# Kernel tuning notes

Hardware: AMD Instinct MI355X
Metric: run time of the kernel (lower is better)

Reference implementation:

```python
import math
import jax, jax.numpy as jnp
import numpy as np

B, H, L = 8, 512, 4096
N = 64 // 2  # d_state//2 complex pairs
DT_MIN, DT_MAX = 1e-3, 0.1


def setup_inputs() -> dict:
    key = jax.random.key(0)
    k_u, k_dt, k_C, k_D, k_W = jax.random.split(key, 5)
    u = jax.random.normal(k_u, (B, H, L), dtype=jnp.float32)
    log_dt = jax.random.uniform(k_dt, (H,), dtype=jnp.float32) * (
        math.log(DT_MAX) - math.log(DT_MIN)) + math.log(DT_MIN)
    log_A_real = jnp.log(0.5 * jnp.ones((H, N), dtype=jnp.float32))
    A_imag = math.pi * jnp.broadcast_to(jnp.arange(N, dtype=jnp.float32), (H, N))
    C = jax.random.normal(k_C, (H, N, 2), dtype=jnp.float32)  # view_as_real of cfloat
    D = jax.random.normal(k_D, (H,), dtype=jnp.float32)
    W_out = jax.random.normal(k_W, (2 * H, H), dtype=jnp.float32) * 0.05  # 1x1 conv weight
    b_out = jnp.zeros((2 * H,), dtype=jnp.float32)
    return {"u": u, "log_dt": log_dt, "log_A_real": log_A_real, "A_imag": A_imag,
            "C": C, "D": D, "W_out": W_out, "b_out": b_out}


def _ssm_kernel(log_dt, log_A_real, A_imag, C, length):
    dt = jnp.exp(log_dt)                             # (H,)
    A = -jnp.exp(log_A_real) + 1j * A_imag           # (H,N) complex
    dtA = A * dt[:, None]                            # (H,N)
    l = jnp.arange(length, dtype=jnp.float32)
    K = jnp.exp(dtA[:, :, None] * l)                 # (H,N,L) complex Vandermonde
    Cc = C[..., 0] + 1j * C[..., 1]                  # (H,N)
    Cs = Cc * (jnp.exp(dtA) - 1.0) / A               # (H,N)
    return 2.0 * jnp.einsum('hn,hnl->hl', Cs, K).real  # (H,L) real kernel


def reference(u, log_dt, log_A_real, A_imag, C, D, W_out, b_out):
    length = u.shape[-1]
    k = _ssm_kernel(log_dt, log_A_real, A_imag, C, length)  # (H,L)
    n_fft = 2 * length
    k_f = jnp.fft.rfft(k, n=n_fft)                   # (H, L+1)
    u_f = jnp.fft.rfft(u, n=n_fft)                   # (B,H,L+1)
    y = jnp.fft.irfft(u_f * k_f, n=n_fft)[..., :length]  # FFT convolution
    y = y + u * D[:, None]                           # D skip connection
    y = jax.nn.gelu(y, approximate=False)            # torch nn.GELU = exact erf
    y = jnp.einsum('oh,bhl->bol', W_out, y) + b_out[:, None]  # 1x1 conv
    a, b = jnp.split(y, 2, axis=-2)                  # GLU over channel dim
    return a * jax.nn.sigmoid(b)
```

## Files before the change

### kernel.cpp

```cpp
#include <hip/hip_runtime.h>
#include <math.h>

constexpr int cB = 8, cH = 512, cL = 4096, cN = 32;
constexpr int cG = 32, cLC = 128;
constexpr int cHN = cH * cN;

constexpr size_t OF_RR  = 0;
constexpr size_t OF_RI  = (size_t)cHN;
constexpr size_t OF_RPR = (size_t)2*cHN;
constexpr size_t OF_RPI = (size_t)3*cHN;
constexpr size_t OF_C2R = (size_t)4*cHN;
constexpr size_t OF_C2I = (size_t)5*cHN;
constexpr size_t OF_DR  = (size_t)6*cHN;
constexpr size_t OF_DI  = (size_t)7*cHN;
constexpr size_t OF_K   = (size_t)8*cHN;
constexpr size_t OF_WP  = OF_K + (size_t)512*128;
constexpr size_t OF_A   = OF_WP + (size_t)1024*512/2;
constexpr size_t OF_V   = OF_A + (size_t)512*128*192/2;
constexpr size_t OF_XP  = OF_V + (size_t)512*64*128/2;
constexpr size_t OF_G   = OF_XP + (size_t)512*256*64/2;
constexpr size_t OF_GT  = OF_A;

typedef __bf16 bf16x8 __attribute__((ext_vector_type(8)));
typedef float  f32x4  __attribute__((ext_vector_type(4)));

static __device__ __forceinline__ ushort f2bf(float x) {
    unsigned u = __float_as_uint(x);
    unsigned r = (u + 0x7fffu + ((u >> 16) & 1u)) >> 16;
    return (ushort)r;
}
static __device__ __forceinline__ float bf2f(ushort v) {
    return __uint_as_float(((unsigned)v) << 16);
}
static __device__ __forceinline__ unsigned pk2(float a, float b) {
    return (unsigned)f2bf(a) | ((unsigned)f2bf(b) << 16);
}
static __device__ __forceinline__ float gelu(float v) {
    return 0.5f * v * (1.0f + erff(v * 0.70710678118654752f));
}
static __device__ __forceinline__ void gload16(const void* g, void* l) {
    __builtin_amdgcn_global_load_lds(
        (const __attribute__((address_space(1))) unsigned*)g,
        (__attribute__((address_space(3))) unsigned*)l, 16, 0, 0);
}

__global__ void k_consts_vmat(const float* __restrict__ log_dt,
                              const float* __restrict__ log_A_real,
                              const float* __restrict__ A_imag,
                              const float* __restrict__ Cin,
                              float* __restrict__ ws,
                              ushort* __restrict__ wsu)
{
    int tid = blockIdx.x * 256 + threadIdx.x;
    if (tid >= cHN) return;
    int h = tid >> 5, n = tid & 31;
    float dt = expf(log_dt[h]);
    float Ar = -expf(log_A_real[tid]);
    float Ai = A_imag[tid];
    float dr = dt * Ar, di = dt * Ai;
    float er = expf(dr);
    float rr = er * cosf(di), ri = er * sinf(di);
    float erL = expf(dr * (float)cLC);
    float diL = di * (float)cLC;
    float rpr = erL * cosf(diL), rpi = erL * sinf(diL);
    float cr = Cin[2*tid], ci = Cin[2*tid+1];
    float nr = rr - 1.0f, ni = ri;
    float inv = 1.0f / (Ar*Ar + Ai*Ai);
    float wr = (nr*Ar + ni*Ai) * inv;
    float wi = (ni*Ar - nr*Ai) * inv;
    float csr = cr*wr - ci*wi;
    float csi = cr*wi + ci*wr;
    ws[OF_RR  + tid] = rr;  ws[OF_RI  + tid] = ri;
    ws[OF_RPR + tid] = rpr; ws[OF_RPI + tid] = rpi;
    ws[OF_C2R + tid] = 2.0f*csr; ws[OF_C2I + tid] = 2.0f*csi;
    ws[OF_DR  + tid] = dr;  ws[OF_DI  + tid] = di;

    float e127 = expf(dr * 127.f), a127 = di * 127.f;
    float pr = e127 * cosf(a127), pi_ = e127 * sinf(a127);
    float rie = expf(-dr);
    float rc = rie * cosf(di), rs = -rie * sinf(di);
    ushort* vre = wsu + 2*OF_V + ((size_t)h*64 + n) * 128;
    ushort* vim = wsu + 2*OF_V + ((size_t)h*64 + 32 + n) * 128;
    for (int j4 = 0; j4 < 128; j4 += 4) {
        ushort4 r4, i4;
        #pragma unroll
        for (int e = 0; e < 4; ++e) {
            ((ushort*)&r4)[e] = f2bf(pr);
            ((ushort*)&i4)[e] = f2bf(pi_);
            float npr = pr*rc - pi_*rs;
            float npi = pr*rs + pi_*rc;
            pr = npr; pi_ = npi;
        }
        *(ushort4*)&vre[j4] = r4;
        *(ushort4*)&vim[j4] = i4;
    }
}

__global__ void k_pack_w(const float* __restrict__ W, ushort* __restrict__ Wp)
{
    int idx = blockIdx.x * 256 + threadIdx.x;
    int base = idx * 4;
    int m = base >> 9;
    int k = base & 511;
    int src = (m & 1) ? (512 + (m >> 1)) : (m >> 1);
    float4 v = *(const float4*)&W[(size_t)src * 512 + k];
    ushort4 o;
    o.x = f2bf(v.x); o.y = f2bf(v.y); o.z = f2bf(v.z); o.w = f2bf(v.w);
    *(ushort4*)&Wp[base] = o;
}

__global__ void k_embt(const float* __restrict__ ws, const float* __restrict__ Dvec,
                       ushort* __restrict__ wsu)
{
    __shared__ float kv[256];
    int t = threadIdx.x;
    int tid = blockIdx.x * 256 + t;
    int h = tid >> 7, l = tid & 127;
    float fl = (float)l, fl1 = (float)(l + 1);
    const float* dr_ = ws + OF_DR + (size_t)h*32;
    const float* di_ = ws + OF_DI + (size_t)h*32;
    const float* c2r_ = ws + OF_C2R + (size_t)h*32;
    const float* c2i_ = ws + OF_C2I + (size_t)h*32;
    ushort* rowA = wsu + 2*OF_A + ((size_t)h*128 + l) * 192;
    float kacc = 0.f;
    for (int n4 = 0; n4 < 32; n4 += 4) {
        ushort4 prq, npq;
        #pragma unroll
        for (int e = 0; e < 4; ++e) {
            int n = n4 + e;
            float dr = dr_[n], di = di_[n], c2r = c2r_[n], c2i = c2i_[n];
            float e0 = expf(dr * fl), a0 = di * fl;
            float c0 = cosf(a0), s0 = sinf(a0);
            kacc += e0 * (c2r*c0 - c2i*s0);
            float e1 = expf(dr * fl1), a1 = di * fl1;
            float c1 = cosf(a1), s1 = sinf(a1);
            ((ushort*)&prq)[e] = f2bf(e1 * (c2r*c1 - c2i*s1));
            ((ushort*)&npq)[e] = f2bf(-e1 * (c2r*s1 + c2i*c1));
        }
        *(ushort4*)&rowA[128 + n4] = prq;
        *(ushort4*)&rowA[160 + n4] = npq;
    }
    kv[t] = kacc;
    __syncthreads();
    const float* krow = kv + ((t >> 7) << 7);
    float Dh = Dvec[h];
    for (int j8 = 0; j8 < 128; j8 += 8) {
        uint4 q;
        unsigned w[4];
        #pragma unroll
        for (int p = 0; p < 4; ++p) {
            int j0 = j8 + 2*p, j1 = j0 + 1;
            float v0 = (j0 <= l) ? krow[l - j0] : 0.f;
            float v1 = (j1 <= l) ? krow[l - j1] : 0.f;
            if (j0 == l) v0 += Dh;
            if (j1 == l) v1 += Dh;
            w[p] = pk2(v0, v1);
        }
        q.x = w[0]; q.y = w[1]; q.z = w[2]; q.w = w[3];
        *(uint4*)&rowA[j8] = q;
    }
}

__global__ __launch_bounds__(256) void k_state_gemm(const float* __restrict__ u,
                                                    const ushort* __restrict__ wsu,
                                                    ushort* __restrict__ xp)
{
    __shared__ ushort Vs[64 * 136];
    __shared__ ushort Bs[256 * 40];
    const int t = threadIdx.x;
    const int h = blockIdx.x;
    const int wn = t >> 6, lane = t & 63;
    const int lm = lane & 15, q = lane >> 4;

    {
        int idx = t * 32;
        int row = idx >> 7, kk = idx & 127;
        const ushort* src = wsu + 2*OF_V + ((size_t)h*64 + row) * 128 + kk;
        uint4 v0 = *(const uint4*)&src[0],  v1 = *(const uint4*)&src[8];
        uint4 v2 = *(const uint4*)&src[16], v3 = *(const uint4*)&src[24];
        ushort* d = (ushort*)Vs + row * 136 + kk;
        *(uint4*)&d[0] = v0; *(uint4*)&d[8] = v1;
        *(uint4*)&d[16] = v2; *(uint4*)&d[24] = v3;
    }

    const int b = t >> 5, c = t & 31;
    f32x4 acc[4][4];
    #pragma unroll
    for (int i = 0; i < 4; ++i)
        #pragma unroll
        for (int j = 0; j < 4; ++j) acc[i][j] = (f32x4){0.f,0.f,0.f,0.f};

    for (int k0 = 0; k0 < 128; k0 += 32) {
        const float* up = u + ((size_t)(b*cH + h)) * cL + (size_t)c*128 + k0;
        float4 f[8];
        #pragma unroll
        for (int e = 0; e < 8; ++e) f[e] = *(const float4*)&up[4*e];
        __syncthreads();
        ushort* d = (ushort*)Bs + t * 40;
        #pragma unroll
        for (int e = 0; e < 4; ++e) {
            uint4 w;
            w.x = pk2(f[2*e].x, f[2*e].y);   w.y = pk2(f[2*e].z, f[2*e].w);
            w.z = pk2(f[2*e+1].x, f[2*e+1].y); w.w = pk2(f[2*e+1].z, f[2*e+1].w);
            *(uint4*)&d[8*e] = w;
        }
        __syncthreads();
        bf16x8 af[4], bfr[4];
        #pragma unroll
        for (int mi = 0; mi < 4; ++mi)
            af[mi] = *(const bf16x8*)&Vs[(16*mi + lm) * 136 + k0 + 8*q];
        #pragma unroll
        for (int ni = 0; ni < 4; ++ni)
            bfr[ni] = *(const bf16x8*)&Bs[(64*wn + 16*ni + lm) * 40 + 8*q];
        #pragma unroll
        for (int mi = 0; mi < 4; ++mi)
            #pragma unroll
            for (int ni = 0; ni < 4; ++ni)
                acc[mi][ni] = __builtin_amdgcn_mfma_f32_16x16x32_bf16(af[mi], bfr[ni], acc[mi][ni], 0,0,0);
    }
    #pragma unroll
    for (int mi = 0; mi < 4; ++mi)
        #pragma unroll
        for (int ni = 0; ni < 4; ++ni) {
            int col = 64*wn + 16*ni + lm;
            int comp = 16*mi + 4*q;
            ushort4 st;
            st.x = f2bf(acc[mi][ni][0]); st.y = f2bf(acc[mi][ni][1]);
            st.z = f2bf(acc[mi][ni][2]); st.w = f2bf(acc[mi][ni][3]);
            *(ushort4*)&xp[((size_t)h*256 + col) * 64 + comp] = st;
        }
}

__global__ __launch_bounds__(256) void k_scan2(const float* __restrict__ ws,
                                               ushort* __restrict__ xp)
{
    int tid = blockIdx.x * 256 + threadIdx.x;
    int n  = tid & 31;
    int bh = tid >> 5;
    int h  = bh & (cH - 1);
    int b  = bh >> 9;
    float rpr = ws[OF_RPR + (size_t)h*32 + n];
    float rpi = ws[OF_RPI + (size_t)h*32 + n];
    float Xr = 0.f, Xi = 0.f;
    ushort* base = xp + ((size_t)h*256 + (size_t)b*32) * 64 + n;
    for (int c = 0; c < cG; ++c) {
        ushort* p = base + (size_t)c * 64;
        float sr = bf2f(p[0]), si = bf2f(p[32]);
        p[0]  = f2bf(Xr);
        p[32] = f2bf(Xi);
        float nXr = fmaf(rpr, Xr, fmaf(-rpi, Xi, sr));
        float nXi = fmaf(rpr, Xi, fmaf(rpi, Xr, si));
        Xr = nXr; Xi = nXi;
    }
}

__global__ __launch_bounds__(256) void k_conv(const float* __restrict__ u,
                                              const ushort* __restrict__ wsu,
                                              ushort* __restrict__ g)
{
    __shared__ ushort As[128 * 40];
    __shared__ ushort Bs[128 * 40];
    const int t = threadIdx.x;
    const int ctile = blockIdx.x;
    const int h = blockIdx.y;
    const int wave = t >> 6, lane = t & 63;
    const int wm = wave & 1, wn = wave >> 1;
    const int lm = lane & 15, q = lane >> 4;

    const int arow = t & 127, ah = t >> 7;
    const int col = arow, half = ah;
    const int gc = ctile * 128 + col;
    const int ub = gc >> 5, uc = gc & 31;

    const ushort* Ab = wsu + 2*OF_A + ((size_t)h*128 + arow) * 192;
    const ushort* xpB = wsu + 2*OF_XP + ((size_t)h*256 + gc) * 64;

    f32x4 acc[4][4];
    #pragma unroll
    for (int i = 0; i < 4; ++i)
        #pragma unroll
        for (int j = 0; j < 4; ++j) acc[i][j] = (f32x4){0.f,0.f,0.f,0.f};

    for (int k0 = 0; k0 < 192; k0 += 32) {
        uint4 a0 = *(const uint4*)&Ab[k0 + 16*ah];
        uint4 a1 = *(const uint4*)&Ab[k0 + 16*ah + 8];
        uint4 b0, b1;
        if (k0 < 128) {
            const float* up = u + ((size_t)(ub*cH + h)) * cL + (size_t)uc*128 + k0 + 16*half;
            float4 f0 = *(const float4*)&up[0],  f1 = *(const float4*)&up[4];
            float4 f2 = *(const float4*)&up[8],  f3 = *(const float4*)&up[12];
            b0.x = pk2(f0.x,f0.y); b0.y = pk2(f0.z,f0.w);
            b0.z = pk2(f1.x,f1.y); b0.w = pk2(f1.z,f1.w);
            b1.x = pk2(f2.x,f2.y); b1.y = pk2(f2.z,f2.w);
            b1.z = pk2(f3.x,f3.y); b1.w = pk2(f3.z,f3.w);
        } else {
            const ushort* xs = xpB + (k0 - 128) + 16*half;
            b0 = *(const uint4*)&xs[0];
            b1 = *(const uint4*)&xs[8];
        }
        __syncthreads();
        *(uint4*)&As[arow*40 + 16*ah]     = a0;
        *(uint4*)&As[arow*40 + 16*ah + 8] = a1;
        *(uint4*)&Bs[col*40 + 16*half]     = b0;
        *(uint4*)&Bs[col*40 + 16*half + 8] = b1;
        __syncthreads();
        bool skip = (wm == 0) && (k0 == 64 || k0 == 96);
        if (!skip) {
            bf16x8 af[4], bfr[4];
            #pragma unroll
            for (int mi = 0; mi < 4; ++mi)
                af[mi] = *(const bf16x8*)&As[(64*wm + 16*mi + lm) * 40 + 8*q];
            #pragma unroll
            for (int ni = 0; ni < 4; ++ni)
                bfr[ni] = *(const bf16x8*)&Bs[(64*wn + 16*ni + lm) * 40 + 8*q];
            #pragma unroll
            for (int mi = 0; mi < 4; ++mi)
                #pragma unroll
                for (int ni = 0; ni < 4; ++ni)
                    acc[mi][ni] = __builtin_amdgcn_mfma_f32_16x16x32_bf16(af[mi], bfr[ni], acc[mi][ni], 0,0,0);
        }
    }
    #pragma unroll
    for (int ni = 0; ni < 4; ++ni) {
        int ocol = ctile*128 + 64*wn + 16*ni + lm;
        int ob = ocol >> 5, oc = ocol & 31;
        ushort* grow = g + ((size_t)(ob*cH + h)) * cL + (size_t)oc*128;
        #pragma unroll
        for (int mi = 0; mi < 4; ++mi) {
            int l = 64*wm + 16*mi + 4*q;
            ushort4 st;
            st.x = f2bf(gelu(acc[mi][ni][0]));
            st.y = f2bf(gelu(acc[mi][ni][1]));
            st.z = f2bf(gelu(acc[mi][ni][2]));
            st.w = f2bf(gelu(acc[mi][ni][3]));
            *(ushort4*)&grow[l] = st;
        }
    }
}

__global__ __launch_bounds__(256) void k_transpose(const ushort* __restrict__ gsrc,
                                                   ushort* __restrict__ gT)
{
    __shared__ ushort tile[64 * 64];
    const int t = threadIdx.x;
    const int b  = blockIdx.z;
    const int h0 = blockIdx.y << 6;
    const int l0 = blockIdx.x << 6;
    const ushort* gb = gsrc + ((size_t)b * cH + h0) * cL + l0;
    const int lb = t & 7;
    #pragma unroll
    for (int half = 0; half < 2; ++half) {
        int r = (t >> 3) + half * 32;
        uint4 v = *(const uint4*)&gb[(size_t)r * cL + lb * 8];
        int sb = lb ^ (r & 7) ^ (r >> 3);
        *(uint4*)&tile[r * 64 + sb * 8] = v;
    }
    __syncthreads();
    ushort* gTb = gT + ((size_t)b * cL + l0) * cH + h0;
    #pragma unroll
    for (int half = 0; half < 2; ++half) {
        int l  = (t >> 3) + half * 32;
        int hb = t & 7;
        ushort vals[8];
        #pragma unroll
        for (int e = 0; e < 8; ++e) {
            int r  = hb * 8 + e;
            int sb = (l >> 3) ^ (r & 7) ^ (r >> 3);
            vals[e] = tile[r * 64 + sb * 8 + (l & 7)];
        }
        *(uint4*)&gTb[(size_t)l * cH + hb * 8] = *(uint4*)vals;
    }
}

__global__ __launch_bounds__(256) void k_gemm2(const ushort* __restrict__ Wp,
                                               const float* __restrict__ bias,
                                               const ushort* __restrict__ gT,
                                               float* __restrict__ out)
{
    __shared__ ushort As[3][128 * 32];
    __shared__ ushort Bs[3][128 * 32];
    const int t    = threadIdx.x;
    const int l0   = blockIdx.x * 128;
    const int by   = blockIdx.y;
    const int b    = blockIdx.z;
    const int wave = t >> 6, lane = t & 63;
    const int wm   = wave & 1, wn = wave >> 1;
    const int lm   = lane & 15, q = lane >> 4;

    const int srow  = lane >> 2;
    const int sw_st = (((lane & 3) ^ ((srow >> 1) & 3)) * 8);
    const int sw_rd = ((q ^ ((lm >> 1) & 3)) * 8);
    const ushort* Ag = Wp + (size_t)(by * 128) * 512;
    const ushort* Bg = gT + ((size_t)b * cL + l0) * 512;

    f32x4 acc[4][4];
    #pragma unroll
    for (int i = 0; i < 4; ++i)
        #pragma unroll
        for (int j = 0; j < 4; ++j)
            acc[i][j] = (f32x4){0.f, 0.f, 0.f, 0.f};

    auto stage = [&](int bi, int kt) {
        const int k0 = kt * 32;
        #pragma unroll
        for (int j = 0; j < 2; ++j) {
            int row = 32*wave + 16*j + srow;
            gload16(Ag + (size_t)row * 512 + k0 + sw_st,
                    (char*)&As[bi][0] + wave*2048 + j*1024);
            gload16(Bg + (size_t)row * 512 + k0 + sw_st,
                    (char*)&Bs[bi][0] + wave*2048 + j*1024);
        }
    };
    auto compute = [&](int bi) {
        bf16x8 af[4], bfr[4];
        #pragma unroll
        for (int mi = 0; mi < 4; ++mi)
            af[mi] = *(const bf16x8*)&As[bi][(64*wm + 16*mi + lm) * 32 + sw_rd];
        #pragma unroll
        for (int ni = 0; ni < 4; ++ni)
            bfr[ni] = *(const bf16x8*)&Bs[bi][(64*wn + 16*ni + lm) * 32 + sw_rd];
        #pragma unroll
        for (int mi = 0; mi < 4; ++mi)
            #pragma unroll
            for (int ni = 0; ni < 4; ++ni)
                acc[mi][ni] = __builtin_amdgcn_mfma_f32_16x16x32_bf16(af[mi], bfr[ni], acc[mi][ni], 0,0,0);
    };

    stage(0, 0);
    stage(1, 1);
    int c0 = 0, c1 = 1, c2 = 2;
    for (int ks = 0; ks < 14; ++ks) {
        stage(c2, ks + 2);
        asm volatile("s_waitcnt vmcnt(8)" ::: "memory");
        __builtin_amdgcn_s_barrier();
        asm volatile("" ::: "memory");
        __builtin_amdgcn_sched_barrier(0);
        compute(c0);
        asm volatile("" ::: "memory");
        __builtin_amdgcn_sched_barrier(0);
        __builtin_amdgcn_s_barrier();
        int tmp = c0; c0 = c1; c1 = c2; c2 = tmp;
    }
    asm volatile("s_waitcnt vmcnt(4)" ::: "memory");
    __builtin_amdgcn_s_barrier();
    asm volatile("" ::: "memory");
    __builtin_amdgcn_sched_barrier(0);
    compute(c0);
    asm volatile("s_waitcnt vmcnt(0)" ::: "memory");
    __builtin_amdgcn_s_barrier();
    asm volatile("" ::: "memory");
    __builtin_amdgcn_sched_barrier(0);
    compute(c1);

    const int obase = by * 64 + 32 * wm;
    #pragma unroll
    for (int mi = 0; mi < 4; ++mi) {
        #pragma unroll
        for (int p = 0; p < 2; ++p) {
            int o = obase + 8*mi + 2*q + p;
            float ba = bias[o], bb = bias[512 + o];
            float* orow = out + ((size_t)b * cH + o) * cL + l0 + 64*wn + lm;
            #pragma unroll
            for (int ni = 0; ni < 4; ++ni) {
                float av = acc[mi][ni][2*p]     + ba;
                float gv = acc[mi][ni][2*p + 1] + bb;
                orow[16 * ni] = av / (1.f + expf(-gv));
            }
        }
    }
}

extern "C" void kernel_launch(void* const* d_in, const int* in_sizes, int n_in,
                              void* d_out, int out_size, void* d_ws, size_t ws_size,
                              hipStream_t stream)
{
    (void)in_sizes; (void)n_in; (void)out_size; (void)ws_size;
    const float* u          = (const float*)d_in[0];
    const float* log_dt     = (const float*)d_in[1];
    const float* log_A_real = (const float*)d_in[2];
    const float* A_imag     = (const float*)d_in[3];
    const float* C          = (const float*)d_in[4];
    const float* D          = (const float*)d_in[5];
    const float* W          = (const float*)d_in[6];
    const float* bias       = (const float*)d_in[7];
    float* out = (float*)d_out;
    float* ws  = (float*)d_ws;
    ushort* wsu = (ushort*)d_ws;
    ushort* Wp  = wsu + 2*OF_WP;
    ushort* xp  = wsu + 2*OF_XP;
    ushort* gbf = wsu + 2*OF_G;
    ushort* gTu = wsu + 2*OF_GT;

    hipLaunchKernelGGL(k_consts_vmat, dim3(cHN/256), dim3(256), 0, stream,
                       log_dt, log_A_real, A_imag, C, ws, wsu);
    hipLaunchKernelGGL(k_pack_w, dim3(1024*512/4/256), dim3(256), 0, stream, W, Wp);
    hipLaunchKernelGGL(k_embt, dim3(512*128/256), dim3(256), 0, stream, ws, D, wsu);
    hipLaunchKernelGGL(k_state_gemm, dim3(512), dim3(256), 0, stream, u, wsu, xp);
    hipLaunchKernelGGL(k_scan2, dim3(cB*cH*cN/256), dim3(256), 0, stream, ws, xp);
    hipLaunchKernelGGL(k_conv, dim3(2, 512), dim3(256), 0, stream, u, wsu, gbf);
    hipLaunchKernelGGL(k_transpose, dim3(cL/64, cH/64, cB), dim3(256), 0, stream, gbf, gTu);
    hipLaunchKernelGGL(k_gemm2, dim3(cL/128, 1024/128, cB), dim3(256), 0, stream,
                       Wp, bias, gTu, out);
}
```

Measured before the change: 288.9 us.

## Enlarge final GEMM tile to 256x128 with 512 threads and K-step 64

The output-projection GEMM now uses 512-thread blocks computing a 256x128 tile with a K step of 64, which halves the grid in the output-channel dimension and halves the number of pipeline iterations. A new XOR swizzle covers 64-wide shared rows, and MFMA sections are wrapped in s_setprio. The aim is more reuse of each B tile and fewer barriers per unit of work. The cost is much more LDS per block (about 144 KB across three stages), which limits occupancy to roughly one block per CU, and a smaller grid (1024 blocks).

```diff
diff --git a/kernel.cpp b/kernel.cpp
--- a/kernel.cpp
+++ b/kernel.cpp
@@ -372,25 +372,26 @@
     }
 }
 
-__global__ __launch_bounds__(256) void k_gemm2(const ushort* __restrict__ Wp,
+__global__ __launch_bounds__(512) void k_gemm2(const ushort* __restrict__ Wp,
                                                const float* __restrict__ bias,
                                                const ushort* __restrict__ gT,
                                                float* __restrict__ out)
 {
-    __shared__ ushort As[3][128 * 32];
-    __shared__ ushort Bs[3][128 * 32];
+    __shared__ ushort As[3][256 * 64];
+    __shared__ ushort Bs[3][128 * 64];
     const int t    = threadIdx.x;
     const int l0   = blockIdx.x * 128;
     const int by   = blockIdx.y;
     const int b    = blockIdx.z;
     const int wave = t >> 6, lane = t & 63;
-    const int wm   = wave & 1, wn = wave >> 1;
+    const int wm   = wave & 3, wn = wave >> 2;
     const int lm   = lane & 15, q = lane >> 4;
 
-    const int srow  = lane >> 2;
-    const int sw_st = (((lane & 3) ^ ((srow >> 1) & 3)) * 8);
-    const int sw_rd = ((q ^ ((lm >> 1) & 3)) * 8);
-    const ushort* Ag = Wp + (size_t)(by * 128) * 512;
+    const int lr8 = lane >> 3;
+    const int lc8 = lane & 7;
+    const int src_sw = ((lc8 ^ lr8) * 8);
+
+    const ushort* Ag = Wp + (size_t)(by * 256) * 512;
     const ushort* Bg = gT + ((size_t)b * cL + l0) * 512;
 
     f32x4 acc[4][4];
@@ -401,58 +402,56 @@
             acc[i][j] = (f32x4){0.f, 0.f, 0.f, 0.f};
 
     auto stage = [&](int bi, int kt) {
-        const int k0 = kt * 32;
+        const int k0 = kt * 64;
+        #pragma unroll
+        for (int j = 0; j < 4; ++j) {
+            int rb = 32*wave + 8*j;
+            gload16(Ag + (size_t)(rb + lr8) * 512 + k0 + src_sw,
+                    (char*)&As[bi][0] + rb * 128);
+        }
         #pragma unroll
         for (int j = 0; j < 2; ++j) {
-            int row = 32*wave + 16*j + srow;
-            gload16(Ag + (size_t)row * 512 + k0 + sw_st,
-                    (char*)&As[bi][0] + wave*2048 + j*1024);
-            gload16(Bg + (size_t)row * 512 + k0 + sw_st,
-                    (char*)&Bs[bi][0] + wave*2048 + j*1024);
+            int rb = 16*wave + 8*j;
+            gload16(Bg + (size_t)(rb + lr8) * 512 + k0 + src_sw,
+                    (char*)&Bs[bi][0] + rb * 128);
         }
     };
     auto compute = [&](int bi) {
-        bf16x8 af[4], bfr[4];
-        #pragma unroll
-        for (int mi = 0; mi < 4; ++mi)
-            af[mi] = *(const bf16x8*)&As[bi][(64*wm + 16*mi + lm) * 32 + sw_rd];
-        #pragma unroll
-        for (int ni = 0; ni < 4; ++ni)
-            bfr[ni] = *(const bf16x8*)&Bs[bi][(64*wn + 16*ni + lm) * 32 + sw_rd];
-        #pragma unroll
-        for (int mi = 0; mi < 4; ++mi)
+        #pragma unroll
+        for (int half = 0; half < 2; ++half) {
+            const int slot = ((q + 4*half) ^ (lm & 7)) * 8;
+            bf16x8 af[4], bfr[4];
+            #pragma unroll
+            for (int mi = 0; mi < 4; ++mi)
+                af[mi] = *(const bf16x8*)&As[bi][(64*wm + 16*mi + lm) * 64 + slot];
             #pragma unroll
             for (int ni = 0; ni < 4; ++ni)
-                acc[mi][ni] = __builtin_amdgcn_mfma_f32_16x16x32_bf16(af[mi], bfr[ni], acc[mi][ni], 0,0,0);
+                bfr[ni] = *(const bf16x8*)&Bs[bi][(64*wn + 16*ni + lm) * 64 + slot];
+            __builtin_amdgcn_s_setprio(1);
+            #pragma unroll
+            for (int mi = 0; mi < 4; ++mi)
+                #pragma unroll
+                for (int ni = 0; ni < 4; ++ni)
+                    acc[mi][ni] = __builtin_amdgcn_mfma_f32_16x16x32_bf16(af[mi], bfr[ni], acc[mi][ni], 0,0,0);
+            __builtin_amdgcn_s_setprio(0);
+        }
     };
 
     stage(0, 0);
     stage(1, 1);
-    int c0 = 0, c1 = 1, c2 = 2;
-    for (int ks = 0; ks < 14; ++ks) {
-        stage(c2, ks + 2);
-        asm volatile("s_waitcnt vmcnt(8)" ::: "memory");
+    for (int it = 0; it < 8; ++it) {
+        if (it < 6) stage((it + 2) % 3, it + 2);
+        if (it < 6)       asm volatile("s_waitcnt vmcnt(12)" ::: "memory");
+        else if (it == 6) asm volatile("s_waitcnt vmcnt(6)"  ::: "memory");
+        else              asm volatile("s_waitcnt vmcnt(0)"  ::: "memory");
         __builtin_amdgcn_s_barrier();
-        asm volatile("" ::: "memory");
         __builtin_amdgcn_sched_barrier(0);
-        compute(c0);
-        asm volatile("" ::: "memory");
+        compute(it % 3);
         __builtin_amdgcn_sched_barrier(0);
         __builtin_amdgcn_s_barrier();
-        int tmp = c0; c0 = c1; c1 = c2; c2 = tmp;
-    }
-    asm volatile("s_waitcnt vmcnt(4)" ::: "memory");
-    __builtin_amdgcn_s_barrier();
-    asm volatile("" ::: "memory");
-    __builtin_amdgcn_sched_barrier(0);
-    compute(c0);
-    asm volatile("s_waitcnt vmcnt(0)" ::: "memory");
-    __builtin_amdgcn_s_barrier();
-    asm volatile("" ::: "memory");
-    __builtin_amdgcn_sched_barrier(0);
-    compute(c1);
-
-    const int obase = by * 64 + 32 * wm;
+    }
+
+    const int obase = by * 128 + 32 * wm;
     #pragma unroll
     for (int mi = 0; mi < 4; ++mi) {
         #pragma unroll
@@ -499,6 +498,6 @@
     hipLaunchKernelGGL(k_scan2, dim3(cB*cH*cN/256), dim3(256), 0, stream, ws, xp);
     hipLaunchKernelGGL(k_conv, dim3(2, 512), dim3(256), 0, stream, u, wsu, gbf);
     hipLaunchKernelGGL(k_transpose, dim3(cL/64, cH/64, cB), dim3(256), 0, stream, gbf, gTu);
-    hipLaunchKernelGGL(k_gemm2, dim3(cL/128, 1024/128, cB), dim3(256), 0, stream,
+    hipLaunchKernelGGL(k_gemm2, dim3(cL/128, 1024/128/2, cB), dim3(512), 0, stream,
                        Wp, bias, gTu, out);
 }
```

After: 329.4 us. 1.14x slower.
